# Kernel tuning notes

Hardware: AMD Instinct MI355X
Metric: run time of the kernel (lower is better)

## Reference

```python
import jax, jax.numpy as jnp
import numpy as np
from jax import lax

INPUT, HIDDEN, OUT = 64, 128, 40
B, T = 256, 512


def _lstm_layer(x, Wih, Whh, bih, bhh):
    # x: [B, T, D]; PyTorch gate order: i, f, g, o in stacked [4H, .] weights
    Bsz = x.shape[0]
    H = Whh.shape[1]
    b = bih + bhh

    def step(carry, xt):
        h, c = carry
        gates = xt @ Wih.T + h @ Whh.T + b  # [B, 4H]
        i, f, g, o = jnp.split(gates, 4, axis=-1)
        i = jax.nn.sigmoid(i)
        f = jax.nn.sigmoid(f)
        g = jnp.tanh(g)
        o = jax.nn.sigmoid(o)
        c = f * c + i * g
        h = o * jnp.tanh(c)
        return (h, c), h

    init = (jnp.zeros((Bsz, H), x.dtype), jnp.zeros((Bsz, H), x.dtype))
    (h_last, _), ys = lax.scan(step, init, jnp.swapaxes(x, 0, 1))
    return jnp.swapaxes(ys, 0, 1), h_last


def setup_inputs() -> dict:
    key = jax.random.key(0)
    ks = jax.random.split(key, 11)
    s_in = 1.0 / np.sqrt(HIDDEN)
    u = lambda k, shp: jax.random.uniform(k, shp, jnp.float32, -s_in, s_in)
    return {
        "x": jax.random.normal(ks[0], (B, T, INPUT), jnp.float32),
        "Wih0": u(ks[1], (4 * HIDDEN, INPUT)),
        "Whh0": u(ks[2], (4 * HIDDEN, HIDDEN)),
        "bih0": u(ks[3], (4 * HIDDEN,)),
        "bhh0": u(ks[4], (4 * HIDDEN,)),
        "Wih1": u(ks[5], (4 * HIDDEN, HIDDEN)),
        "Whh1": u(ks[6], (4 * HIDDEN, HIDDEN)),
        "bih1": u(ks[7], (4 * HIDDEN,)),
        "bhh1": u(ks[8], (4 * HIDDEN,)),
        "Wfc": u(ks[9], (OUT, HIDDEN)),
        "bfc": u(ks[10], (OUT,)),
    }


def reference(x, Wih0, Whh0, bih0, bhh0, Wih1, Whh1, bih1, bhh1, Wfc, bfc):
    y0, _ = _lstm_layer(x, Wih0, Whh0, bih0, bhh0)        # [B, T, H]
    _, h_last = _lstm_layer(y0, Wih1, Whh1, bih1, bhh1)   # [B, H] == y[:, -1]
    return h_last @ Wfc.T + bfc                            # [B, 40]
```

## Files before the change

kernel.cpp:

```cpp
#include <hip/hip_runtime.h>

#define BATCH 256
#define TLEN  512
#define DIN   64
#define HID   128
#define NOUT  40

typedef _Float16 f16x8 __attribute__((ext_vector_type(8)));
typedef _Float16 f16x4 __attribute__((ext_vector_type(4)));
typedef float    f32x4 __attribute__((ext_vector_type(4)));

#define MFMA16(a, b, c) __builtin_amdgcn_mfma_f32_16x16x32_f16((a), (b), (c), 0, 0, 0)

#define BARRIER() do {                                      \
    asm volatile("s_waitcnt lgkmcnt(0)" ::: "memory");      \
    __builtin_amdgcn_s_barrier();                           \
} while (0)

static __device__ __forceinline__ f16x8 pack8(float4 a, float4 b) {
    f16x8 v;
    v[0] = (_Float16)a.x; v[1] = (_Float16)a.y; v[2] = (_Float16)a.z; v[3] = (_Float16)a.w;
    v[4] = (_Float16)b.x; v[5] = (_Float16)b.y; v[6] = (_Float16)b.z; v[7] = (_Float16)b.w;
    return v;
}
static __device__ __forceinline__ float sig_(float x) {
    return __builtin_amdgcn_rcpf(1.0f + __expf(-x));
}
static __device__ __forceinline__ float tanh_(float x) {
    return fmaf(-2.0f, __builtin_amdgcn_rcpf(__expf(2.0f * x) + 1.0f), 1.0f);
}

#define LD8(base, g, K, kt) pack8(*(const float4*)((base) + (size_t)(g) * (K) + (kt) * 32 + kg * 8), \
                                  *(const float4*)((base) + (size_t)(g) * (K) + (kt) * 32 + kg * 8 + 4))

__global__ void __attribute__((amdgpu_flat_work_group_size(512, 512), amdgpu_waves_per_eu(2, 2)))
lstm_l0(const float* __restrict__ x,
        const float* __restrict__ Wih, const float* __restrict__ Whh,
        const float* __restrict__ bih, const float* __restrict__ bhh,
        float* __restrict__ hstate, float* __restrict__ cstate,
        _Float16* __restrict__ y0, int t0, int t1)
{
    const int b    = blockIdx.x;
    const int tid  = threadIdx.x;
    const int lane = tid & 63, wave = tid >> 6;
    const int col  = lane & 15, kg = lane >> 4;
    const int hid  = wave * 16 + col;

    __shared__ __align__(16) _Float16 x_lds[2][DIN];
    __shared__ __align__(16) _Float16 h_lds[2][HID];

    f16x8 Wx00 = LD8(Wih, 0 * HID + hid, DIN, 0), Wx01 = LD8(Wih, 0 * HID + hid, DIN, 1);
    f16x8 Wx10 = LD8(Wih, 1 * HID + hid, DIN, 0), Wx11 = LD8(Wih, 1 * HID + hid, DIN, 1);
    f16x8 Wx20 = LD8(Wih, 2 * HID + hid, DIN, 0), Wx21 = LD8(Wih, 2 * HID + hid, DIN, 1);
    f16x8 Wx30 = LD8(Wih, 3 * HID + hid, DIN, 0), Wx31 = LD8(Wih, 3 * HID + hid, DIN, 1);
    f16x8 Wh00 = LD8(Whh, 0 * HID + hid, HID, 0), Wh01 = LD8(Whh, 0 * HID + hid, HID, 1);
    f16x8 Wh02 = LD8(Whh, 0 * HID + hid, HID, 2), Wh03 = LD8(Whh, 0 * HID + hid, HID, 3);
    f16x8 Wh10 = LD8(Whh, 1 * HID + hid, HID, 0), Wh11 = LD8(Whh, 1 * HID + hid, HID, 1);
    f16x8 Wh12 = LD8(Whh, 1 * HID + hid, HID, 2), Wh13 = LD8(Whh, 1 * HID + hid, HID, 3);
    f16x8 Wh20 = LD8(Whh, 2 * HID + hid, HID, 0), Wh21 = LD8(Whh, 2 * HID + hid, HID, 1);
    f16x8 Wh22 = LD8(Whh, 2 * HID + hid, HID, 2), Wh23 = LD8(Whh, 2 * HID + hid, HID, 3);
    f16x8 Wh30 = LD8(Whh, 3 * HID + hid, HID, 0), Wh31 = LD8(Whh, 3 * HID + hid, HID, 1);
    f16x8 Wh32 = LD8(Whh, 3 * HID + hid, HID, 2), Wh33 = LD8(Whh, 3 * HID + hid, HID, 3);
    asm("" : "+a"(Wx00), "+a"(Wx01), "+a"(Wx10), "+a"(Wx11),
             "+a"(Wx20), "+a"(Wx21), "+a"(Wx30), "+a"(Wx31));
    asm("" : "+a"(Wh00), "+a"(Wh01), "+a"(Wh02), "+a"(Wh03),
             "+a"(Wh10), "+a"(Wh11), "+a"(Wh12), "+a"(Wh13));
    asm("" : "+a"(Wh20), "+a"(Wh21), "+a"(Wh22), "+a"(Wh23),
             "+a"(Wh30), "+a"(Wh31), "+a"(Wh32), "+a"(Wh33));

    const float bs0 = bih[0 * HID + hid] + bhh[0 * HID + hid];
    const float bs1 = bih[1 * HID + hid] + bhh[1 * HID + hid];
    const float bs2 = bih[2 * HID + hid] + bhh[2 * HID + hid];
    const float bs3 = bih[3 * HID + hid] + bhh[3 * HID + hid];
    const f32x4 z4 = {0.f, 0.f, 0.f, 0.f};

    float cc = cstate[(size_t)b * HID + hid];
    float hv = hstate[(size_t)b * HID + hid];
    if (kg == 0) h_lds[0][hid] = (_Float16)hv;

    const float4* xrow = (const float4*)(x + (size_t)b * TLEN * DIN);
    const int lk = tid - 448;
    const bool ldr = ((unsigned)lk < 16u);
    float4 xpfA = make_float4(0, 0, 0, 0), xpfB = xpfA;
    if (ldr) {
        int g0 = t0,     g1 = t0 + 1, g2 = t0 + 2, g3 = t0 + 3;
        if (g1 > TLEN - 1) g1 = TLEN - 1;
        if (g2 > TLEN - 1) g2 = TLEN - 1;
        if (g3 > TLEN - 1) g3 = TLEN - 1;
        float4 v0 = xrow[(size_t)g0 * (DIN / 4) + lk];
        float4 v1 = xrow[(size_t)g1 * (DIN / 4) + lk];
        f16x4 p;
        p[0] = (_Float16)v0.x; p[1] = (_Float16)v0.y; p[2] = (_Float16)v0.z; p[3] = (_Float16)v0.w;
        *(f16x4*)&x_lds[0][lk * 4] = p;
        p[0] = (_Float16)v1.x; p[1] = (_Float16)v1.y; p[2] = (_Float16)v1.z; p[3] = (_Float16)v1.w;
        *(f16x4*)&x_lds[1][lk * 4] = p;
        xpfA = xrow[(size_t)g2 * (DIN / 4) + lk];
        xpfB = xrow[(size_t)g3 * (DIN / 4) + lk];
    }
    BARRIER();

    f32x4 U0, U1, U2, U3, V0, V1, V2, V3;
    {
        f16x8 p0 = *(const f16x8*)&x_lds[0][kg * 8];
        f16x8 p1 = *(const f16x8*)&x_lds[0][32 + kg * 8];
        U0 = MFMA16(p0, Wx00, z4); U1 = MFMA16(p0, Wx10, z4);
        U2 = MFMA16(p0, Wx20, z4); U3 = MFMA16(p0, Wx30, z4);
        U0 = MFMA16(p1, Wx01, U0); U1 = MFMA16(p1, Wx11, U1);
        U2 = MFMA16(p1, Wx21, U2); U3 = MFMA16(p1, Wx31, U3);
    }
    BARRIER();

#define L0_STEP(T, P, XPF, C0, C1, C2, C3, N0, N1, N2, N3) do {                  \
    if (ldr) {                                                                   \
        f16x4 pw; pw[0] = (_Float16)XPF.x; pw[1] = (_Float16)XPF.y;              \
        pw[2] = (_Float16)XPF.z; pw[3] = (_Float16)XPF.w;                        \
        *(f16x4*)&x_lds[P][lk * 4] = pw;                                         \
        int tn = (T) + 4; if (tn > TLEN - 1) tn = TLEN - 1;                      \
        XPF = xrow[(size_t)tn * (DIN / 4) + lk];                                 \
    }                                                                            \
    f16x8 ha0 = *(const f16x8*)&h_lds[P][kg * 8];                                \
    f16x8 ha1 = *(const f16x8*)&h_lds[P][32 + kg * 8];                           \
    f16x8 ha2 = *(const f16x8*)&h_lds[P][64 + kg * 8];                           \
    f16x8 ha3 = *(const f16x8*)&h_lds[P][96 + kg * 8];                           \
    f16x8 xa0 = *(const f16x8*)&x_lds[(P) ^ 1][kg * 8];                          \
    f16x8 xa1 = *(const f16x8*)&x_lds[(P) ^ 1][32 + kg * 8];                     \
    f32x4 a0 = MFMA16(ha0, Wh00, C0), a1 = MFMA16(ha0, Wh10, C1);                \
    f32x4 a2 = MFMA16(ha0, Wh20, C2), a3 = MFMA16(ha0, Wh30, C3);                \
    a0 = MFMA16(ha1, Wh01, a0); a1 = MFMA16(ha1, Wh11, a1);                      \
    a2 = MFMA16(ha1, Wh21, a2); a3 = MFMA16(ha1, Wh31, a3);                      \
    a0 = MFMA16(ha2, Wh02, a0); a1 = MFMA16(ha2, Wh12, a1);                      \
    a2 = MFMA16(ha2, Wh22, a2); a3 = MFMA16(ha2, Wh32, a3);                      \
    a0 = MFMA16(ha3, Wh03, a0); a1 = MFMA16(ha3, Wh13, a1);                      \
    a2 = MFMA16(ha3, Wh23, a2); a3 = MFMA16(ha3, Wh33, a3);                      \
    N0 = MFMA16(xa0, Wx00, z4); N1 = MFMA16(xa0, Wx10, z4);                      \
    N2 = MFMA16(xa0, Wx20, z4); N3 = MFMA16(xa0, Wx30, z4);                      \
    N0 = MFMA16(xa1, Wx01, N0); N1 = MFMA16(xa1, Wx11, N1);                      \
    N2 = MFMA16(xa1, Wx21, N2); N3 = MFMA16(xa1, Wx31, N3);                      \
    float iv = sig_(a0[0] + bs0), fv = sig_(a1[0] + bs1);                        \
    float gv = tanh_(a2[0] + bs2), ov = sig_(a3[0] + bs3);                       \
    cc = fmaf(fv, cc, iv * gv);                                                  \
    hv = ov * tanh_(cc);                                                         \
    _Float16 hh = (_Float16)hv;                                                  \
    if (kg == 0) {                                                               \
        h_lds[(P) ^ 1][hid] = hh;                                                \
        y0[((size_t)((T) - t0) * BATCH + b) * HID + hid] = hh;                   \
    }                                                                            \
    BARRIER();                                                                   \
} while (0)

    const int nt = t1 - t0;
    for (int s = 0; s + 1 < nt; s += 2) {
        L0_STEP(t0 + s,     0, xpfA, U0, U1, U2, U3, V0, V1, V2, V3);
        L0_STEP(t0 + s + 1, 1, xpfB, V0, V1, V2, V3, U0, U1, U2, U3);
    }
#undef L0_STEP

    if (kg == 0) {
        cstate[(size_t)b * HID + hid] = cc;
        hstate[(size_t)b * HID + hid] = hv;
    }
}

__global__ void __attribute__((amdgpu_flat_work_group_size(512, 512), amdgpu_waves_per_eu(2, 2)))
lstm_l1(const _Float16* __restrict__ y0in,
        const float* __restrict__ Wih, const float* __restrict__ Whh,
        const float* __restrict__ bih, const float* __restrict__ bhh,
        float* __restrict__ hstate, float* __restrict__ cstate,
        int t0, int t1)
{
    const int b    = blockIdx.x;
    const int tid  = threadIdx.x;
    const int lane = tid & 63, wave = tid >> 6;
    const int col  = lane & 15, kg = lane >> 4;
    const int hid  = wave * 16 + col;

    __shared__ __align__(16) _Float16 y_lds[2][HID];
    __shared__ __align__(16) _Float16 h_lds[2][HID];

    f16x8 Wy00 = LD8(Wih, 0 * HID + hid, HID, 0), Wy01 = LD8(Wih, 0 * HID + hid, HID, 1);
    f16x8 Wy02 = LD8(Wih, 0 * HID + hid, HID, 2), Wy03 = LD8(Wih, 0 * HID + hid, HID, 3);
    f16x8 Wy10 = LD8(Wih, 1 * HID + hid, HID, 0), Wy11 = LD8(Wih, 1 * HID + hid, HID, 1);
    f16x8 Wy12 = LD8(Wih, 1 * HID + hid, HID, 2), Wy13 = LD8(Wih, 1 * HID + hid, HID, 3);
    f16x8 Wy20 = LD8(Wih, 2 * HID + hid, HID, 0), Wy21 = LD8(Wih, 2 * HID + hid, HID, 1);
    f16x8 Wy22 = LD8(Wih, 2 * HID + hid, HID, 2), Wy23 = LD8(Wih, 2 * HID + hid, HID, 3);
    f16x8 Wy30 = LD8(Wih, 3 * HID + hid, HID, 0), Wy31 = LD8(Wih, 3 * HID + hid, HID, 1);
    f16x8 Wy32 = LD8(Wih, 3 * HID + hid, HID, 2), Wy33 = LD8(Wih, 3 * HID + hid, HID, 3);
    f16x8 Wh00 = LD8(Whh, 0 * HID + hid, HID, 0), Wh01 = LD8(Whh, 0 * HID + hid, HID, 1);
    f16x8 Wh02 = LD8(Whh, 0 * HID + hid, HID, 2), Wh03 = LD8(Whh, 0 * HID + hid, HID, 3);
    f16x8 Wh10 = LD8(Whh, 1 * HID + hid, HID, 0), Wh11 = LD8(Whh, 1 * HID + hid, HID, 1);
    f16x8 Wh12 = LD8(Whh, 1 * HID + hid, HID, 2), Wh13 = LD8(Whh, 1 * HID + hid, HID, 3);
    f16x8 Wh20 = LD8(Whh, 2 * HID + hid, HID, 0), Wh21 = LD8(Whh, 2 * HID + hid, HID, 1);
    f16x8 Wh22 = LD8(Whh, 2 * HID + hid, HID, 2), Wh23 = LD8(Whh, 2 * HID + hid, HID, 3);
    f16x8 Wh30 = LD8(Whh, 3 * HID + hid, HID, 0), Wh31 = LD8(Whh, 3 * HID + hid, HID, 1);
    f16x8 Wh32 = LD8(Whh, 3 * HID + hid, HID, 2), Wh33 = LD8(Whh, 3 * HID + hid, HID, 3);
    asm("" : "+a"(Wy00), "+a"(Wy01), "+a"(Wy02), "+a"(Wy03),
             "+a"(Wy10), "+a"(Wy11), "+a"(Wy12), "+a"(Wy13));
    asm("" : "+a"(Wy20), "+a"(Wy21), "+a"(Wy22), "+a"(Wy23),
             "+a"(Wy30), "+a"(Wy31), "+a"(Wy32), "+a"(Wy33));
    asm("" : "+a"(Wh00), "+a"(Wh01), "+a"(Wh02), "+a"(Wh03),
             "+a"(Wh10), "+a"(Wh11), "+a"(Wh12), "+a"(Wh13));
    asm("" : "+a"(Wh20), "+a"(Wh21), "+a"(Wh22), "+a"(Wh23),
             "+a"(Wh30), "+a"(Wh31), "+a"(Wh32), "+a"(Wh33));

    const float bs0 = bih[0 * HID + hid] + bhh[0 * HID + hid];
    const float bs1 = bih[1 * HID + hid] + bhh[1 * HID + hid];
    const float bs2 = bih[2 * HID + hid] + bhh[2 * HID + hid];
    const float bs3 = bih[3 * HID + hid] + bhh[3 * HID + hid];
    const f32x4 z4 = {0.f, 0.f, 0.f, 0.f};

    float cc = cstate[(size_t)b * HID + hid];
    float hv = hstate[(size_t)b * HID + hid];
    if (kg == 0) h_lds[0][hid] = (_Float16)hv;

    const uint4* yrow = (const uint4*)(y0in);
    const int lk = tid - 448;
    const bool ldr = ((unsigned)lk < 16u);
    const int nt = t1 - t0;
    uint4 ypfA = make_uint4(0, 0, 0, 0), ypfB = ypfA;
    if (ldr) {
        int i1 = 1 < nt - 1 ? 1 : nt - 1;
        int i2 = 2 < nt - 1 ? 2 : nt - 1;
        int i3 = 3 < nt - 1 ? 3 : nt - 1;
        *(uint4*)&y_lds[0][lk * 8] = yrow[((size_t)0 * BATCH + b) * (HID / 8) + lk];
        *(uint4*)&y_lds[1][lk * 8] = yrow[((size_t)i1 * BATCH + b) * (HID / 8) + lk];
        ypfA = yrow[((size_t)i2 * BATCH + b) * (HID / 8) + lk];
        ypfB = yrow[((size_t)i3 * BATCH + b) * (HID / 8) + lk];
    }
    BARRIER();

    f32x4 U0, U1, U2, U3, V0, V1, V2, V3;
    {
        f16x8 p0 = *(const f16x8*)&y_lds[0][kg * 8];
        f16x8 p1 = *(const f16x8*)&y_lds[0][32 + kg * 8];
        f16x8 p2 = *(const f16x8*)&y_lds[0][64 + kg * 8];
        f16x8 p3 = *(const f16x8*)&y_lds[0][96 + kg * 8];
        U0 = MFMA16(p0, Wy00, z4); U1 = MFMA16(p0, Wy10, z4);
        U2 = MFMA16(p0, Wy20, z4); U3 = MFMA16(p0, Wy30, z4);
        U0 = MFMA16(p1, Wy01, U0); U1 = MFMA16(p1, Wy11, U1);
        U2 = MFMA16(p1, Wy21, U2); U3 = MFMA16(p1, Wy31, U3);
        U0 = MFMA16(p2, Wy02, U0); U1 = MFMA16(p2, Wy12, U1);
        U2 = MFMA16(p2, Wy22, U2); U3 = MFMA16(p2, Wy32, U3);
        U0 = MFMA16(p3, Wy03, U0); U1 = MFMA16(p3, Wy13, U1);
        U2 = MFMA16(p3, Wy23, U2); U3 = MFMA16(p3, Wy33, U3);
    }
    BARRIER();

#define L1_STEP(REL, P, YPF, C0, C1, C2, C3, N0, N1, N2, N3) do {                \
    if (ldr) {                                                                   \
        *(uint4*)&y_lds[P][lk * 8] = YPF;                                        \
        int rn = (REL) + 4; if (rn > nt - 1) rn = nt - 1;                        \
        YPF = yrow[((size_t)rn * BATCH + b) * (HID / 8) + lk];                   \
    }                                                                            \
    f16x8 ha0 = *(const f16x8*)&h_lds[P][kg * 8];                                \
    f16x8 ha1 = *(const f16x8*)&h_lds[P][32 + kg * 8];                           \
    f16x8 ha2 = *(const f16x8*)&h_lds[P][64 + kg * 8];                           \
    f16x8 ha3 = *(const f16x8*)&h_lds[P][96 + kg * 8];                           \
    f16x8 ya0 = *(const f16x8*)&y_lds[(P) ^ 1][kg * 8];                          \
    f16x8 ya1 = *(const f16x8*)&y_lds[(P) ^ 1][32 + kg * 8];                     \
    f16x8 ya2 = *(const f16x8*)&y_lds[(P) ^ 1][64 + kg * 8];                     \
    f16x8 ya3 = *(const f16x8*)&y_lds[(P) ^ 1][96 + kg * 8];                     \
    f32x4 a0 = MFMA16(ha0, Wh00, C0), a1 = MFMA16(ha0, Wh10, C1);                \
    f32x4 a2 = MFMA16(ha0, Wh20, C2), a3 = MFMA16(ha0, Wh30, C3);                \
    a0 = MFMA16(ha1, Wh01, a0); a1 = MFMA16(ha1, Wh11, a1);                      \
    a2 = MFMA16(ha1, Wh21, a2); a3 = MFMA16(ha1, Wh31, a3);                      \
    a0 = MFMA16(ha2, Wh02, a0); a1 = MFMA16(ha2, Wh12, a1);                      \
    a2 = MFMA16(ha2, Wh22, a2); a3 = MFMA16(ha2, Wh32, a3);                      \
    a0 = MFMA16(ha3, Wh03, a0); a1 = MFMA16(ha3, Wh13, a1);                      \
    a2 = MFMA16(ha3, Wh23, a2); a3 = MFMA16(ha3, Wh33, a3);                      \
    N0 = MFMA16(ya0, Wy00, z4); N1 = MFMA16(ya0, Wy10, z4);                      \
    N2 = MFMA16(ya0, Wy20, z4); N3 = MFMA16(ya0, Wy30, z4);                      \
    N0 = MFMA16(ya1, Wy01, N0); N1 = MFMA16(ya1, Wy11, N1);                      \
    N2 = MFMA16(ya1, Wy21, N2); N3 = MFMA16(ya1, Wy31, N3);                      \
    N0 = MFMA16(ya2, Wy02, N0); N1 = MFMA16(ya2, Wy12, N1);                      \
    N2 = MFMA16(ya2, Wy22, N2); N3 = MFMA16(ya2, Wy32, N3);                      \
    N0 = MFMA16(ya3, Wy03, N0); N1 = MFMA16(ya3, Wy13, N1);                      \
    N2 = MFMA16(ya3, Wy23, N2); N3 = MFMA16(ya3, Wy33, N3);                      \
    float iv = sig_(a0[0] + bs0), fv = sig_(a1[0] + bs1);                        \
    float gv = tanh_(a2[0] + bs2), ov = sig_(a3[0] + bs3);                       \
    cc = fmaf(fv, cc, iv * gv);                                                  \
    hv = ov * tanh_(cc);                                                         \
    if (kg == 0) h_lds[(P) ^ 1][hid] = (_Float16)hv;                             \
    BARRIER();                                                                   \
} while (0)

    for (int s = 0; s + 1 < nt; s += 2) {
        L1_STEP(s,     0, ypfA, U0, U1, U2, U3, V0, V1, V2, V3);
        L1_STEP(s + 1, 1, ypfB, V0, V1, V2, V3, U0, U1, U2, U3);
    }
#undef L1_STEP

    if (kg == 0) {
        cstate[(size_t)b * HID + hid] = cc;
        hstate[(size_t)b * HID + hid] = hv;
    }
}

__global__ __launch_bounds__(128) void fc_kernel(
    const float* __restrict__ h1, const float* __restrict__ Wfc,
    const float* __restrict__ bfc, float* __restrict__ out)
{
    const int b = blockIdx.x;
    const int o = threadIdx.x;
    __shared__ float hs[HID];
    hs[o] = h1[(size_t)b * HID + o];
    __syncthreads();
    if (o < NOUT) {
        const float4* w  = reinterpret_cast<const float4*>(Wfc + (size_t)o * HID);
        const float4* hv = reinterpret_cast<const float4*>(hs);
        float acc = bfc[o];
        #pragma unroll
        for (int q = 0; q < HID / 4; ++q) {
            float4 wv = w[q]; float4 h4 = hv[q];
            acc = fmaf(wv.x, h4.x, fmaf(wv.y, h4.y, fmaf(wv.z, h4.z, fmaf(wv.w, h4.w, acc))));
        }
        out[(size_t)b * NOUT + o] = acc;
    }
}

extern "C" void kernel_launch(void* const* d_in, const int* in_sizes, int n_in,
                              void* d_out, int out_size, void* d_ws, size_t ws_size,
                              hipStream_t stream) {
    const float* x    = (const float*)d_in[0];
    const float* Wih0 = (const float*)d_in[1];
    const float* Whh0 = (const float*)d_in[2];
    const float* bih0 = (const float*)d_in[3];
    const float* bhh0 = (const float*)d_in[4];
    const float* Wih1 = (const float*)d_in[5];
    const float* Whh1 = (const float*)d_in[6];
    const float* bih1 = (const float*)d_in[7];
    const float* bhh1 = (const float*)d_in[8];
    const float* Wfc  = (const float*)d_in[9];
    const float* bfc  = (const float*)d_in[10];
    float* out = (float*)d_out;

    float* hst0 = (float*)d_ws;
    float* cst0 = hst0 + BATCH * HID;
    float* hst1 = cst0 + BATCH * HID;
    float* cst1 = hst1 + BATCH * HID;
    _Float16* y0 = (_Float16*)(cst1 + BATCH * HID);

    const size_t stateBytes = (size_t)4 * BATCH * HID * sizeof(float);
    size_t avail = ws_size > stateBytes ? ws_size - stateBytes : 0;
    int Tc = (int)(avail / ((size_t)BATCH * HID * 2));
    if (Tc > TLEN) Tc = TLEN;
    Tc &= ~1;
    if (Tc < 2) Tc = 2;

    hipMemsetAsync(d_ws, 0, stateBytes, stream);

    for (int t0 = 0; t0 < TLEN; t0 += Tc) {
        int t1 = t0 + Tc; if (t1 > TLEN) t1 = TLEN;
        lstm_l0<<<BATCH, 512, 0, stream>>>(x, Wih0, Whh0, bih0, bhh0, hst0, cst0, y0, t0, t1);
        lstm_l1<<<BATCH, 512, 0, stream>>>(y0, Wih1, Whh1, bih1, bhh1, hst1, cst1, t0, t1);
    }
    fc_kernel<<<BATCH, 128, 0, stream>>>(hst1, Wfc, bfc, out);
}
```

Before: 650.8 us.

## Batch input projections over 16-step chunks via MFMA time-as-rows, stage in LDS

```diff
diff --git a/kernel.cpp b/kernel.cpp
--- a/kernel.cpp
+++ b/kernel.cpp
@@ -5,9 +5,9 @@
 #define DIN   64
 #define HID   128
 #define NOUT  40
+#define SC    16
 
 typedef _Float16 f16x8 __attribute__((ext_vector_type(8)));
-typedef _Float16 f16x4 __attribute__((ext_vector_type(4)));
 typedef float    f32x4 __attribute__((ext_vector_type(4)));
 
 #define MFMA16(a, b, c) __builtin_amdgcn_mfma_f32_16x16x32_f16((a), (b), (c), 0, 0, 0)
@@ -29,9 +29,32 @@
 static __device__ __forceinline__ float tanh_(float x) {
     return fmaf(-2.0f, __builtin_amdgcn_rcpf(__expf(2.0f * x) + 1.0f), 1.0f);
 }
+static __device__ __forceinline__ f32x4 splat4(float v) { return (f32x4){v, v, v, v}; }
 
 #define LD8(base, g, K, kt) pack8(*(const float4*)((base) + (size_t)(g) * (K) + (kt) * 32 + kg * 8), \
                                   *(const float4*)((base) + (size_t)(g) * (K) + (kt) * 32 + kg * 8 + 4))
+
+#define H_STEP_CORE(SL, P)                                                      \
+    f32x4 xi = *(const f32x4*)&xacc[((SL) * HID + hid) * 4];                    \
+    const _Float16* hb = &h_lds[P][0];                                          \
+    f16x8 h0 = *(const f16x8*)(hb + kg * 8);                                    \
+    f16x8 h1 = *(const f16x8*)(hb + 32 + kg * 8);                               \
+    f16x8 h2 = *(const f16x8*)(hb + 64 + kg * 8);                               \
+    f16x8 h3 = *(const f16x8*)(hb + 96 + kg * 8);                               \
+    f32x4 a0 = MFMA16(h0, Wh00, xi);                                            \
+    f32x4 a1 = MFMA16(h0, Wh10, splat4(xi[1]));                                 \
+    f32x4 a2 = MFMA16(h0, Wh20, splat4(xi[2]));                                 \
+    f32x4 a3 = MFMA16(h0, Wh30, splat4(xi[3]));                                 \
+    a0 = MFMA16(h1, Wh01, a0); a1 = MFMA16(h1, Wh11, a1);                       \
+    a2 = MFMA16(h1, Wh21, a2); a3 = MFMA16(h1, Wh31, a3);                       \
+    a0 = MFMA16(h2, Wh02, a0); a1 = MFMA16(h2, Wh12, a1);                       \
+    a2 = MFMA16(h2, Wh22, a2); a3 = MFMA16(h2, Wh32, a3);                       \
+    a0 = MFMA16(h3, Wh03, a0); a1 = MFMA16(h3, Wh13, a1);                       \
+    a2 = MFMA16(h3, Wh23, a2); a3 = MFMA16(h3, Wh33, a3);                       \
+    float iv = sig_(a0[0]), fv = sig_(a1[0]);                                   \
+    float gv = tanh_(a2[0]), ov = sig_(a3[0]);                                  \
+    cc = fmaf(fv, cc, iv * gv);                                                 \
+    hv = ov * tanh_(cc);
 
 __global__ void __attribute__((amdgpu_flat_work_group_size(512, 512), amdgpu_waves_per_eu(2, 2)))
 lstm_l0(const float* __restrict__ x,
@@ -42,11 +65,12 @@
 {
     const int b    = blockIdx.x;
     const int tid  = threadIdx.x;
-    const int lane = tid & 63, wave = tid >> 6;
+    const int lane = tid & 63;
+    const int wave = tid >> 6;
     const int col  = lane & 15, kg = lane >> 4;
     const int hid  = wave * 16 + col;
 
-    __shared__ __align__(16) _Float16 x_lds[2][DIN];
+    __shared__ __align__(16) float    xacc[SC * HID * 4];
     __shared__ __align__(16) _Float16 h_lds[2][HID];
 
     f16x8 Wx00 = LD8(Wih, 0 * HID + hid, DIN, 0), Wx01 = LD8(Wih, 0 * HID + hid, DIN, 1);
@@ -72,89 +96,52 @@
     const float bs1 = bih[1 * HID + hid] + bhh[1 * HID + hid];
     const float bs2 = bih[2 * HID + hid] + bhh[2 * HID + hid];
     const float bs3 = bih[3 * HID + hid] + bhh[3 * HID + hid];
-    const f32x4 z4 = {0.f, 0.f, 0.f, 0.f};
 
     float cc = cstate[(size_t)b * HID + hid];
     float hv = hstate[(size_t)b * HID + hid];
     if (kg == 0) h_lds[0][hid] = (_Float16)hv;
 
-    const float4* xrow = (const float4*)(x + (size_t)b * TLEN * DIN);
-    const int lk = tid - 448;
-    const bool ldr = ((unsigned)lk < 16u);
-    float4 xpfA = make_float4(0, 0, 0, 0), xpfB = xpfA;
-    if (ldr) {
-        int g0 = t0,     g1 = t0 + 1, g2 = t0 + 2, g3 = t0 + 3;
-        if (g1 > TLEN - 1) g1 = TLEN - 1;
-        if (g2 > TLEN - 1) g2 = TLEN - 1;
-        if (g3 > TLEN - 1) g3 = TLEN - 1;
-        float4 v0 = xrow[(size_t)g0 * (DIN / 4) + lk];
-        float4 v1 = xrow[(size_t)g1 * (DIN / 4) + lk];
-        f16x4 p;
-        p[0] = (_Float16)v0.x; p[1] = (_Float16)v0.y; p[2] = (_Float16)v0.z; p[3] = (_Float16)v0.w;
-        *(f16x4*)&x_lds[0][lk * 4] = p;
-        p[0] = (_Float16)v1.x; p[1] = (_Float16)v1.y; p[2] = (_Float16)v1.z; p[3] = (_Float16)v1.w;
-        *(f16x4*)&x_lds[1][lk * 4] = p;
-        xpfA = xrow[(size_t)g2 * (DIN / 4) + lk];
-        xpfB = xrow[(size_t)g3 * (DIN / 4) + lk];
-    }
-    BARRIER();
-
-    f32x4 U0, U1, U2, U3, V0, V1, V2, V3;
-    {
-        f16x8 p0 = *(const f16x8*)&x_lds[0][kg * 8];
-        f16x8 p1 = *(const f16x8*)&x_lds[0][32 + kg * 8];
-        U0 = MFMA16(p0, Wx00, z4); U1 = MFMA16(p0, Wx10, z4);
-        U2 = MFMA16(p0, Wx20, z4); U3 = MFMA16(p0, Wx30, z4);
-        U0 = MFMA16(p1, Wx01, U0); U1 = MFMA16(p1, Wx11, U1);
-        U2 = MFMA16(p1, Wx21, U2); U3 = MFMA16(p1, Wx31, U3);
-    }
-    BARRIER();
-
-#define L0_STEP(T, P, XPF, C0, C1, C2, C3, N0, N1, N2, N3) do {                  \
-    if (ldr) {                                                                   \
-        f16x4 pw; pw[0] = (_Float16)XPF.x; pw[1] = (_Float16)XPF.y;              \
-        pw[2] = (_Float16)XPF.z; pw[3] = (_Float16)XPF.w;                        \
-        *(f16x4*)&x_lds[P][lk * 4] = pw;                                         \
-        int tn = (T) + 4; if (tn > TLEN - 1) tn = TLEN - 1;                      \
-        XPF = xrow[(size_t)tn * (DIN / 4) + lk];                                 \
-    }                                                                            \
-    f16x8 ha0 = *(const f16x8*)&h_lds[P][kg * 8];                                \
-    f16x8 ha1 = *(const f16x8*)&h_lds[P][32 + kg * 8];                           \
-    f16x8 ha2 = *(const f16x8*)&h_lds[P][64 + kg * 8];                           \
-    f16x8 ha3 = *(const f16x8*)&h_lds[P][96 + kg * 8];                           \
-    f16x8 xa0 = *(const f16x8*)&x_lds[(P) ^ 1][kg * 8];                          \
-    f16x8 xa1 = *(const f16x8*)&x_lds[(P) ^ 1][32 + kg * 8];                     \
-    f32x4 a0 = MFMA16(ha0, Wh00, C0), a1 = MFMA16(ha0, Wh10, C1);                \
-    f32x4 a2 = MFMA16(ha0, Wh20, C2), a3 = MFMA16(ha0, Wh30, C3);                \
-    a0 = MFMA16(ha1, Wh01, a0); a1 = MFMA16(ha1, Wh11, a1);                      \
-    a2 = MFMA16(ha1, Wh21, a2); a3 = MFMA16(ha1, Wh31, a3);                      \
-    a0 = MFMA16(ha2, Wh02, a0); a1 = MFMA16(ha2, Wh12, a1);                      \
-    a2 = MFMA16(ha2, Wh22, a2); a3 = MFMA16(ha2, Wh32, a3);                      \
-    a0 = MFMA16(ha3, Wh03, a0); a1 = MFMA16(ha3, Wh13, a1);                      \
-    a2 = MFMA16(ha3, Wh23, a2); a3 = MFMA16(ha3, Wh33, a3);                      \
-    N0 = MFMA16(xa0, Wx00, z4); N1 = MFMA16(xa0, Wx10, z4);                      \
-    N2 = MFMA16(xa0, Wx20, z4); N3 = MFMA16(xa0, Wx30, z4);                      \
-    N0 = MFMA16(xa1, Wx01, N0); N1 = MFMA16(xa1, Wx11, N1);                      \
-    N2 = MFMA16(xa1, Wx21, N2); N3 = MFMA16(xa1, Wx31, N3);                      \
-    float iv = sig_(a0[0] + bs0), fv = sig_(a1[0] + bs1);                        \
-    float gv = tanh_(a2[0] + bs2), ov = sig_(a3[0] + bs3);                       \
-    cc = fmaf(fv, cc, iv * gv);                                                  \
-    hv = ov * tanh_(cc);                                                         \
-    _Float16 hh = (_Float16)hv;                                                  \
-    if (kg == 0) {                                                               \
-        h_lds[(P) ^ 1][hid] = hh;                                                \
-        y0[((size_t)((T) - t0) * BATCH + b) * HID + hid] = hh;                   \
-    }                                                                            \
-    BARRIER();                                                                   \
-} while (0)
+    const float* xA = x + (size_t)b * TLEN * DIN + (size_t)col * DIN + kg * 8;
+    _Float16* y0p = y0 + (size_t)b * HID + hid;
 
     const int nt = t1 - t0;
-    for (int s = 0; s + 1 < nt; s += 2) {
-        L0_STEP(t0 + s,     0, xpfA, U0, U1, U2, U3, V0, V1, V2, V3);
-        L0_STEP(t0 + s + 1, 1, xpfB, V0, V1, V2, V3, U0, U1, U2, U3);
-    }
-#undef L0_STEP
-
+    for (int sc = 0; sc < nt; sc += SC) {
+        {
+            const float* pa = xA + (size_t)(t0 + sc) * DIN;
+            f16x8 A0 = pack8(*(const float4*)pa,        *(const float4*)(pa + 4));
+            f16x8 A1 = pack8(*(const float4*)(pa + 32), *(const float4*)(pa + 36));
+            f32x4 g0 = splat4(bs0), g1 = splat4(bs1), g2 = splat4(bs2), g3 = splat4(bs3);
+            g0 = MFMA16(A0, Wx00, g0); g1 = MFMA16(A0, Wx10, g1);
+            g2 = MFMA16(A0, Wx20, g2); g3 = MFMA16(A0, Wx30, g3);
+            g0 = MFMA16(A1, Wx01, g0); g1 = MFMA16(A1, Wx11, g1);
+            g2 = MFMA16(A1, Wx21, g2); g3 = MFMA16(A1, Wx31, g3);
+            #pragma unroll
+            for (int r = 0; r < 4; ++r) {
+                const int tl = kg * 4 + r;
+                float* d = &xacc[(tl * HID + hid) * 4];
+                d[0] = g0[r]; d[1] = g1[r]; d[2] = g2[r]; d[3] = g3[r];
+            }
+        }
+        BARRIER();
+        for (int s = 0; s < SC; s += 2) {
+            {
+                H_STEP_CORE(s, 0)
+                if (kg == 0) {
+                    h_lds[1][hid] = (_Float16)hv;
+                    y0p[(size_t)(sc + s) * (BATCH * HID)] = (_Float16)hv;
+                }
+                BARRIER();
+            }
+            {
+                H_STEP_CORE(s + 1, 1)
+                if (kg == 0) {
+                    h_lds[0][hid] = (_Float16)hv;
+                    y0p[(size_t)(sc + s + 1) * (BATCH * HID)] = (_Float16)hv;
+                }
+                BARRIER();
+            }
+        }
+    }
     if (kg == 0) {
         cstate[(size_t)b * HID + hid] = cc;
         hstate[(size_t)b * HID + hid] = hv;
@@ -170,21 +157,14 @@
 {
     const int b    = blockIdx.x;
     const int tid  = threadIdx.x;
-    const int lane = tid & 63, wave = tid >> 6;
+    const int lane = tid & 63;
+    const int wave = tid >> 6;
     const int col  = lane & 15, kg = lane >> 4;
     const int hid  = wave * 16 + col;
 
-    __shared__ __align__(16) _Float16 y_lds[2][HID];
+    __shared__ __align__(16) float    xacc[SC * HID * 4];
     __shared__ __align__(16) _Float16 h_lds[2][HID];
 
-    f16x8 Wy00 = LD8(Wih, 0 * HID + hid, HID, 0), Wy01 = LD8(Wih, 0 * HID + hid, HID, 1);
-    f16x8 Wy02 = LD8(Wih, 0 * HID + hid, HID, 2), Wy03 = LD8(Wih, 0 * HID + hid, HID, 3);
-    f16x8 Wy10 = LD8(Wih, 1 * HID + hid, HID, 0), Wy11 = LD8(Wih, 1 * HID + hid, HID, 1);
-    f16x8 Wy12 = LD8(Wih, 1 * HID + hid, HID, 2), Wy13 = LD8(Wih, 1 * HID + hid, HID, 3);
-    f16x8 Wy20 = LD8(Wih, 2 * HID + hid, HID, 0), Wy21 = LD8(Wih, 2 * HID + hid, HID, 1);
-    f16x8 Wy22 = LD8(Wih, 2 * HID + hid, HID, 2), Wy23 = LD8(Wih, 2 * HID + hid, HID, 3);
-    f16x8 Wy30 = LD8(Wih, 3 * HID + hid, HID, 0), Wy31 = LD8(Wih, 3 * HID + hid, HID, 1);
-    f16x8 Wy32 = LD8(Wih, 3 * HID + hid, HID, 2), Wy33 = LD8(Wih, 3 * HID + hid, HID, 3);
     f16x8 Wh00 = LD8(Whh, 0 * HID + hid, HID, 0), Wh01 = LD8(Whh, 0 * HID + hid, HID, 1);
     f16x8 Wh02 = LD8(Whh, 0 * HID + hid, HID, 2), Wh03 = LD8(Whh, 0 * HID + hid, HID, 3);
     f16x8 Wh10 = LD8(Whh, 1 * HID + hid, HID, 0), Wh11 = LD8(Whh, 1 * HID + hid, HID, 1);
@@ -193,10 +173,6 @@
     f16x8 Wh22 = LD8(Whh, 2 * HID + hid, HID, 2), Wh23 = LD8(Whh, 2 * HID + hid, HID, 3);
     f16x8 Wh30 = LD8(Whh, 3 * HID + hid, HID, 0), Wh31 = LD8(Whh, 3 * HID + hid, HID, 1);
     f16x8 Wh32 = LD8(Whh, 3 * HID + hid, HID, 2), Wh33 = LD8(Whh, 3 * HID + hid, HID, 3);
-    asm("" : "+a"(Wy00), "+a"(Wy01), "+a"(Wy02), "+a"(Wy03),
-             "+a"(Wy10), "+a"(Wy11), "+a"(Wy12), "+a"(Wy13));
-    asm("" : "+a"(Wy20), "+a"(Wy21), "+a"(Wy22), "+a"(Wy23),
-             "+a"(Wy30), "+a"(Wy31), "+a"(Wy32), "+a"(Wy33));
     asm("" : "+a"(Wh00), "+a"(Wh01), "+a"(Wh02), "+a"(Wh03),
              "+a"(Wh10), "+a"(Wh11), "+a"(Wh12), "+a"(Wh13));
     asm("" : "+a"(Wh20), "+a"(Wh21), "+a"(Wh22), "+a"(Wh23),
@@ -206,89 +182,59 @@
     const float bs1 = bih[1 * HID + hid] + bhh[1 * HID + hid];
     const float bs2 = bih[2 * HID + hid] + bhh[2 * HID + hid];
     const float bs3 = bih[3 * HID + hid] + bhh[3 * HID + hid];
-    const f32x4 z4 = {0.f, 0.f, 0.f, 0.f};
 
     float cc = cstate[(size_t)b * HID + hid];
     float hv = hstate[(size_t)b * HID + hid];
     if (kg == 0) h_lds[0][hid] = (_Float16)hv;
 
-    const uint4* yrow = (const uint4*)(y0in);
-    const int lk = tid - 448;
-    const bool ldr = ((unsigned)lk < 16u);
+    const _Float16* yA = y0in + ((size_t)col * BATCH + b) * HID + kg * 8;
+
     const int nt = t1 - t0;
-    uint4 ypfA = make_uint4(0, 0, 0, 0), ypfB = ypfA;
-    if (ldr) {
-        int i1 = 1 < nt - 1 ? 1 : nt - 1;
-        int i2 = 2 < nt - 1 ? 2 : nt - 1;
-        int i3 = 3 < nt - 1 ? 3 : nt - 1;
-        *(uint4*)&y_lds[0][lk * 8] = yrow[((size_t)0 * BATCH + b) * (HID / 8) + lk];
-        *(uint4*)&y_lds[1][lk * 8] = yrow[((size_t)i1 * BATCH + b) * (HID / 8) + lk];
-        ypfA = yrow[((size_t)i2 * BATCH + b) * (HID / 8) + lk];
-        ypfB = yrow[((size_t)i3 * BATCH + b) * (HID / 8) + lk];
-    }
-    BARRIER();
-
-    f32x4 U0, U1, U2, U3, V0, V1, V2, V3;
-    {
-        f16x8 p0 = *(const f16x8*)&y_lds[0][kg * 8];
-        f16x8 p1 = *(const f16x8*)&y_lds[0][32 + kg * 8];
-        f16x8 p2 = *(const f16x8*)&y_lds[0][64 + kg * 8];
-        f16x8 p3 = *(const f16x8*)&y_lds[0][96 + kg * 8];
-        U0 = MFMA16(p0, Wy00, z4); U1 = MFMA16(p0, Wy10, z4);
-        U2 = MFMA16(p0, Wy20, z4); U3 = MFMA16(p0, Wy30, z4);
-        U0 = MFMA16(p1, Wy01, U0); U1 = MFMA16(p1, Wy11, U1);
-        U2 = MFMA16(p1, Wy21, U2); U3 = MFMA16(p1, Wy31, U3);
-        U0 = MFMA16(p2, Wy02, U0); U1 = MFMA16(p2, Wy12, U1);
-        U2 = MFMA16(p2, Wy22, U2); U3 = MFMA16(p2, Wy32, U3);
-        U0 = MFMA16(p3, Wy03, U0); U1 = MFMA16(p3, Wy13, U1);
-        U2 = MFMA16(p3, Wy23, U2); U3 = MFMA16(p3, Wy33, U3);
-    }
-    BARRIER();
-
-#define L1_STEP(REL, P, YPF, C0, C1, C2, C3, N0, N1, N2, N3) do {                \
-    if (ldr) {                                                                   \
-        *(uint4*)&y_lds[P][lk * 8] = YPF;                                        \
-        int rn = (REL) + 4; if (rn > nt - 1) rn = nt - 1;                        \
-        YPF = yrow[((size_t)rn * BATCH + b) * (HID / 8) + lk];                   \
-    }                                                                            \
-    f16x8 ha0 = *(const f16x8*)&h_lds[P][kg * 8];                                \
-    f16x8 ha1 = *(const f16x8*)&h_lds[P][32 + kg * 8];                           \
-    f16x8 ha2 = *(const f16x8*)&h_lds[P][64 + kg * 8];                           \
-    f16x8 ha3 = *(const f16x8*)&h_lds[P][96 + kg * 8];                           \
-    f16x8 ya0 = *(const f16x8*)&y_lds[(P) ^ 1][kg * 8];                          \
-    f16x8 ya1 = *(const f16x8*)&y_lds[(P) ^ 1][32 + kg * 8];                     \
-    f16x8 ya2 = *(const f16x8*)&y_lds[(P) ^ 1][64 + kg * 8];                     \
-    f16x8 ya3 = *(const f16x8*)&y_lds[(P) ^ 1][96 + kg * 8];                     \
-    f32x4 a0 = MFMA16(ha0, Wh00, C0), a1 = MFMA16(ha0, Wh10, C1);                \
-    f32x4 a2 = MFMA16(ha0, Wh20, C2), a3 = MFMA16(ha0, Wh30, C3);                \
-    a0 = MFMA16(ha1, Wh01, a0); a1 = MFMA16(ha1, Wh11, a1);                      \
-    a2 = MFMA16(ha1, Wh21, a2); a3 = MFMA16(ha1, Wh31, a3);                      \
-    a0 = MFMA16(ha2, Wh02, a0); a1 = MFMA16(ha2, Wh12, a1);                      \
-    a2 = MFMA16(ha2, Wh22, a2); a3 = MFMA16(ha2, Wh32, a3);                      \
-    a0 = MFMA16(ha3, Wh03, a0); a1 = MFMA16(ha3, Wh13, a1);                      \
-    a2 = MFMA16(ha3, Wh23, a2); a3 = MFMA16(ha3, Wh33, a3);                      \
-    N0 = MFMA16(ya0, Wy00, z4); N1 = MFMA16(ya0, Wy10, z4);                      \
-    N2 = MFMA16(ya0, Wy20, z4); N3 = MFMA16(ya0, Wy30, z4);                      \
-    N0 = MFMA16(ya1, Wy01, N0); N1 = MFMA16(ya1, Wy11, N1);                      \
-    N2 = MFMA16(ya1, Wy21, N2); N3 = MFMA16(ya1, Wy31, N3);                      \
-    N0 = MFMA16(ya2, Wy02, N0); N1 = MFMA16(ya2, Wy12, N1);                      \
-    N2 = MFMA16(ya2, Wy22, N2); N3 = MFMA16(ya2, Wy32, N3);                      \
-    N0 = MFMA16(ya3, Wy03, N0); N1 = MFMA16(ya3, Wy13, N1);                      \
-    N2 = MFMA16(ya3, Wy23, N2); N3 = MFMA16(ya3, Wy33, N3);                      \
-    float iv = sig_(a0[0] + bs0), fv = sig_(a1[0] + bs1);                        \
-    float gv = tanh_(a2[0] + bs2), ov = sig_(a3[0] + bs3);                       \
-    cc = fmaf(fv, cc, iv * gv);                                                  \
-    hv = ov * tanh_(cc);                                                         \
-    if (kg == 0) h_lds[(P) ^ 1][hid] = (_Float16)hv;                             \
-    BARRIER();                                                                   \
-} while (0)
-
-    for (int s = 0; s + 1 < nt; s += 2) {
-        L1_STEP(s,     0, ypfA, U0, U1, U2, U3, V0, V1, V2, V3);
-        L1_STEP(s + 1, 1, ypfB, V0, V1, V2, V3, U0, U1, U2, U3);
-    }
-#undef L1_STEP
-
+    for (int sc = 0; sc < nt; sc += SC) {
+        {
+            f16x8 Wy00 = LD8(Wih, 0 * HID + hid, HID, 0), Wy01 = LD8(Wih, 0 * HID + hid, HID, 1);
+            f16x8 Wy02 = LD8(Wih, 0 * HID + hid, HID, 2), Wy03 = LD8(Wih, 0 * HID + hid, HID, 3);
+            f16x8 Wy10 = LD8(Wih, 1 * HID + hid, HID, 0), Wy11 = LD8(Wih, 1 * HID + hid, HID, 1);
+            f16x8 Wy12 = LD8(Wih, 1 * HID + hid, HID, 2), Wy13 = LD8(Wih, 1 * HID + hid, HID, 3);
+            f16x8 Wy20 = LD8(Wih, 2 * HID + hid, HID, 0), Wy21 = LD8(Wih, 2 * HID + hid, HID, 1);
+            f16x8 Wy22 = LD8(Wih, 2 * HID + hid, HID, 2), Wy23 = LD8(Wih, 2 * HID + hid, HID, 3);
+            f16x8 Wy30 = LD8(Wih, 3 * HID + hid, HID, 0), Wy31 = LD8(Wih, 3 * HID + hid, HID, 1);
+            f16x8 Wy32 = LD8(Wih, 3 * HID + hid, HID, 2), Wy33 = LD8(Wih, 3 * HID + hid, HID, 3);
+            const _Float16* pa = yA + (size_t)sc * (BATCH * HID);
+            f16x8 A0 = *(const f16x8*)(pa);
+            f16x8 A1 = *(const f16x8*)(pa + 32);
+            f16x8 A2 = *(const f16x8*)(pa + 64);
+            f16x8 A3 = *(const f16x8*)(pa + 96);
+            f32x4 g0 = splat4(bs0), g1 = splat4(bs1), g2 = splat4(bs2), g3 = splat4(bs3);
+            g0 = MFMA16(A0, Wy00, g0); g1 = MFMA16(A0, Wy10, g1);
+            g2 = MFMA16(A0, Wy20, g2); g3 = MFMA16(A0, Wy30, g3);
+            g0 = MFMA16(A1, Wy01, g0); g1 = MFMA16(A1, Wy11, g1);
+            g2 = MFMA16(A1, Wy21, g2); g3 = MFMA16(A1, Wy31, g3);
+            g0 = MFMA16(A2, Wy02, g0); g1 = MFMA16(A2, Wy12, g1);
+            g2 = MFMA16(A2, Wy22, g2); g3 = MFMA16(A2, Wy32, g3);
+            g0 = MFMA16(A3, Wy03, g0); g1 = MFMA16(A3, Wy13, g1);
+            g2 = MFMA16(A3, Wy23, g2); g3 = MFMA16(A3, Wy33, g3);
+            #pragma unroll
+            for (int r = 0; r < 4; ++r) {
+                const int tl = kg * 4 + r;
+                float* d = &xacc[(tl * HID + hid) * 4];
+                d[0] = g0[r]; d[1] = g1[r]; d[2] = g2[r]; d[3] = g3[r];
+            }
+        }
+        BARRIER();
+        for (int s = 0; s < SC; s += 2) {
+            {
+                H_STEP_CORE(s, 0)
+                if (kg == 0) h_lds[1][hid] = (_Float16)hv;
+                BARRIER();
+            }
+            {
+                H_STEP_CORE(s + 1, 1)
+                if (kg == 0) h_lds[0][hid] = (_Float16)hv;
+                BARRIER();
+            }
+        }
+    }
     if (kg == 0) {
         cstate[(size_t)b * HID + hid] = cc;
         hstate[(size_t)b * HID + hid] = hv;
@@ -343,8 +289,8 @@
     size_t avail = ws_size > stateBytes ? ws_size - stateBytes : 0;
     int Tc = (int)(avail / ((size_t)BATCH * HID * 2));
     if (Tc > TLEN) Tc = TLEN;
-    Tc &= ~1;
-    if (Tc < 2) Tc = 2;
+    Tc &= ~(SC - 1);
+    if (Tc < SC) Tc = SC;
 
     hipMemsetAsync(d_ws, 0, stateBytes, stream);
 
```

New measurement: 578.3 us. -11.1%, faster.
